# Kernel optimization log

Measured on AMD Instinct MI355X. Metric: run time of the kernel, lower is better.

## Reference

```python
import jax, jax.numpy as jnp
import numpy as np

N = 50000
E = 800000
IN_CH = 128
HID = 64
H1 = 4  # heads in gat1
NEG_SLOPE = 0.2


def _gat_layer(x, src, dst, W, a_src, a_dst, bias, heads, ch):
    # x: [N, F_in]; W: [F_in, heads*ch]; a_src/a_dst: [heads, ch]; bias: [heads*ch]
    n = x.shape[0]
    h = (x @ W).reshape(n, heads, ch)                       # [N, H, C]
    alpha_src = jnp.einsum('nhc,hc->nh', h, a_src)          # [N, H]
    alpha_dst = jnp.einsum('nhc,hc->nh', h, a_dst)          # [N, H]
    e = jax.nn.leaky_relu(alpha_src[src] + alpha_dst[dst], NEG_SLOPE)  # [E, H]
    # segment softmax over incoming edges of each destination node
    m = jax.ops.segment_max(e, dst, num_segments=n)         # [N, H]
    ex = jnp.exp(e - m[dst])                                # [E, H]
    denom = jax.ops.segment_sum(ex, dst, num_segments=n)    # [N, H]
    alpha = ex / (denom[dst] + 1e-16)                       # [E, H]
    out = jax.ops.segment_sum(alpha[:, :, None] * h[src], dst, num_segments=n)  # [N, H, C]
    return out.reshape(n, heads * ch) + bias


def setup_inputs() -> dict:
    key = jax.random.key(0)
    ks = jax.random.split(key, 12)
    x = jax.random.normal(ks[0], (N, IN_CH), dtype=jnp.float32)
    edge_index = jax.random.randint(ks[1], (2, E), 0, N, dtype=jnp.int64)
    s1 = 1.0 / np.sqrt(IN_CH)
    s2 = 1.0 / np.sqrt(H1 * HID)
    s3 = 1.0 / np.sqrt(HID)
    return {
        'x': x,
        'edge_index': edge_index,
        'W1': jax.random.uniform(ks[2], (IN_CH, H1 * HID), jnp.float32, -s1, s1),
        'att_src1': jax.random.uniform(ks[3], (H1, HID), jnp.float32, -s1, s1),
        'att_dst1': jax.random.uniform(ks[4], (H1, HID), jnp.float32, -s1, s1),
        'b1': jnp.zeros((H1 * HID,), jnp.float32),
        'W2': jax.random.uniform(ks[5], (H1 * HID, HID), jnp.float32, -s2, s2),
        'att_src2': jax.random.uniform(ks[6], (1, HID), jnp.float32, -s2, s2),
        'att_dst2': jax.random.uniform(ks[7], (1, HID), jnp.float32, -s2, s2),
        'b2': jnp.zeros((HID,), jnp.float32),
        'W_out': jax.random.uniform(ks[8], (HID, 1), jnp.float32, -s3, s3),
        'b_out': jnp.zeros((1,), jnp.float32),
    }


def reference(x, edge_index, W1, att_src1, att_dst1, b1, W2, att_src2, att_dst2, b2, W_out, b_out):
    # add self-loops (PyG GATConv default)
    loops = jnp.arange(N, dtype=edge_index.dtype)
    src = jnp.concatenate([edge_index[0], loops])
    dst = jnp.concatenate([edge_index[1], loops])
    h = jax.nn.relu(_gat_layer(x, src, dst, W1, att_src1, att_dst1, b1, H1, HID))
    h = jax.nn.relu(_gat_layer(h, src, dst, W2, att_src2, att_dst2, b2, 1, HID))
    return (h @ W_out + b_out).squeeze(-1)  # [N]
```

## Files before the change

### kernel.cpp

```cpp
#include <hip/hip_runtime.h>
#include <hip/hip_bf16.h>
#include <math.h>

#define N_NODES 50000
#define N_EDGES 800000
#define EE_TOTAL (N_EDGES + N_NODES)
#define CAP 64

#define GEMM1_BLOCKS ((N_NODES + 63) / 64)
#define SCAT_BLOCKS ((EE_TOTAL + 1023) / 1024)
#define FUSED_BLOCKS (GEMM1_BLOCKS + SCAT_BLOCKS)
#define AGG1_BLOCKS 25000

typedef __attribute__((ext_vector_type(8))) short bf16x8;
typedef __attribute__((ext_vector_type(4))) float f32x4;

__device__ __forceinline__ float bf2f(unsigned short s) {
  return __uint_as_float((unsigned)s << 16);
}
__device__ __forceinline__ unsigned short f2bf(float f) {
  unsigned u = __float_as_uint(f);
  return (unsigned short)((u + 0x7FFFu + ((u >> 16) & 1u)) >> 16);
}
__device__ __forceinline__ float lrelu(float e) { return e > 0.f ? e : 0.2f * e; }

__global__ void prep_kernel(const float* __restrict__ W1, const float* __restrict__ W2,
                            unsigned short* __restrict__ W1t, unsigned short* __restrict__ W2t,
                            int* __restrict__ counts) {
  int i = blockIdx.x * blockDim.x + threadIdx.x;
  if (i < N_NODES) counts[i] = 0;
  if (i < 256 * 128) W1t[i] = f2bf(W1[(i & 127) * 256 + (i >> 7)]);
  if (i < 64 * 256) W2t[i] = f2bf(W2[(i & 255) * 64 + (i >> 8)]);
}

__device__ __forceinline__ void scatter_body(int sid, int t,
                                             const int* __restrict__ src,
                                             const int* __restrict__ dst,
                                             int* __restrict__ counts,
                                             unsigned short* __restrict__ col) {
  int base = sid * 1024 + t * 4;
  int ss[4], dd[4];
#pragma unroll
  for (int k = 0; k < 4; ++k) {
    int i = base + k;
    if (i < N_EDGES) { ss[k] = src[i]; dd[k] = dst[i]; }
    else if (i < EE_TOTAL) { ss[k] = i - N_EDGES; dd[k] = ss[k]; }
    else { ss[k] = 0; dd[k] = -1; }
  }
#pragma unroll
  for (int k = 0; k < 4; ++k) {
    if (dd[k] >= 0) {
      int pos = atomicAdd(&counts[dd[k]], 1);
      if (pos < CAP) col[(size_t)dd[k] * CAP + pos] = (unsigned short)ss[k];
    }
  }
}

__global__ __launch_bounds__(256) void fused_kernel(const int* __restrict__ src,
                                                    const int* __restrict__ dst,
                                                    int* __restrict__ counts,
                                                    unsigned short* __restrict__ col,
                                                    const float* __restrict__ A,
                                                    const unsigned short* __restrict__ Bt,
                                                    unsigned short* __restrict__ Cb,
                                                    const float* __restrict__ att_s,
                                                    const float* __restrict__ att_d,
                                                    float* __restrict__ as_out,
                                                    float* __restrict__ ad_out) {
  __shared__ unsigned short Bs[256 * 128];
  int b = blockIdx.x;
  int t = threadIdx.x;
  bool is_gemm;
  int id;
  if (b < 2 * GEMM1_BLOCKS) { is_gemm = (b & 1) == 0; id = b >> 1; }
  else { is_gemm = false; id = b - GEMM1_BLOCKS; }

  if (!is_gemm) {
    scatter_body(id, t, src, dst, counts, col);
    return;
  }

  const int M = N_NODES;
  int lane = t & 63, w = t >> 6;
  int row0 = id * 64;
#pragma unroll
  for (int i = 0; i < 16; ++i) {
    int idx = i * 256 + t;
    int n = idx >> 4;
    uint4 v = ((const uint4*)Bt)[idx];
    int byte = (idx * 16) ^ ((n & 7) << 4);
    *(uint4*)((char*)Bs + byte) = v;
  }
  __syncthreads();
  int rl = lane & 15, kg = lane >> 4;
  f32x4 acc[4][4] = {};
  for (int ks = 0; ks < 4; ++ks) {
    bf16x8 af[4], bfr[4];
#pragma unroll
    for (int rb = 0; rb < 4; ++rb) {
      int row = row0 + rb * 16 + rl;
      float4 v0 = make_float4(0.f, 0.f, 0.f, 0.f), v1 = v0;
      if (row < M) {
        const float* p = A + (size_t)row * 128 + ks * 32 + kg * 8;
        v0 = *(const float4*)p;
        v1 = *(const float4*)(p + 4);
      }
      bf16x8 a;
      a[0] = (short)f2bf(v0.x); a[1] = (short)f2bf(v0.y);
      a[2] = (short)f2bf(v0.z); a[3] = (short)f2bf(v0.w);
      a[4] = (short)f2bf(v1.x); a[5] = (short)f2bf(v1.y);
      a[6] = (short)f2bf(v1.z); a[7] = (short)f2bf(v1.w);
      af[rb] = a;
    }
#pragma unroll
    for (int cb = 0; cb < 4; ++cb) {
      int n = w * 64 + cb * 16 + rl;
      int byte = (n * 256 + ks * 64 + kg * 16) ^ ((n & 7) << 4);
      bfr[cb] = *(const bf16x8*)((char*)Bs + byte);
    }
#pragma unroll
    for (int rb = 0; rb < 4; ++rb)
#pragma unroll
      for (int cb = 0; cb < 4; ++cb)
        acc[rb][cb] = __builtin_amdgcn_mfma_f32_16x16x32_bf16(af[rb], bfr[cb], acc[rb][cb], 0, 0, 0);
  }
  float asv[4], adv[4];
#pragma unroll
  for (int cb = 0; cb < 4; ++cb) {
    int c = w * 64 + cb * 16 + rl;
    asv[cb] = att_s[c];
    adv[cb] = att_d[c];
  }
#pragma unroll
  for (int rb = 0; rb < 4; ++rb) {
#pragma unroll
    for (int r = 0; r < 4; ++r) {
      int row = row0 + rb * 16 + kg * 4 + r;
      bool ok = row < M;
      float sp = 0.f, dp = 0.f;
#pragma unroll
      for (int cb = 0; cb < 4; ++cb) {
        float v = acc[rb][cb][r];
        if (ok) Cb[(size_t)row * 256 + w * 64 + cb * 16 + rl] = f2bf(v);
        sp += v * asv[cb];
        dp += v * adv[cb];
      }
#pragma unroll
      for (int off = 1; off < 16; off <<= 1) {
        sp += __shfl_xor(sp, off, 64);
        dp += __shfl_xor(dp, off, 64);
      }
      if (ok && rl == 0) {
        as_out[w * M + row] = sp;
        ad_out[w * M + row] = dp;
      }
    }
  }
}

__global__ __launch_bounds__(256) void gemm2_kernel(const unsigned short* __restrict__ A,
                                                    const unsigned short* __restrict__ Bt,
                                                    unsigned short* __restrict__ Cb,
                                                    const float* __restrict__ att_s,
                                                    const float* __restrict__ att_d,
                                                    float* __restrict__ as_out,
                                                    float* __restrict__ ad_out) {
  __shared__ unsigned short Bs[64 * 256];
  const int M = N_NODES;
  int t = threadIdx.x;
  int lane = t & 63, w = t >> 6;
  int row0 = blockIdx.x * 64;
#pragma unroll
  for (int i = 0; i < 8; ++i) {
    int idx = i * 256 + t;
    int n = idx >> 5;
    uint4 v = ((const uint4*)Bt)[idx];
    int byte = (idx * 16) ^ ((n & 7) << 4);
    *(uint4*)((char*)Bs + byte) = v;
  }
  __syncthreads();
  int rl = lane & 15, kg = lane >> 4;
  int arow = row0 + w * 16 + rl;
  f32x4 acc[4] = {};
  for (int ks = 0; ks < 8; ++ks) {
    bf16x8 a = {};
    if (arow < M) a = *(const bf16x8*)(A + (size_t)arow * 256 + ks * 32 + kg * 8);
#pragma unroll
    for (int cb = 0; cb < 4; ++cb) {
      int n = cb * 16 + rl;
      int byte = (n * 512 + ks * 64 + kg * 16) ^ ((n & 7) << 4);
      bf16x8 bfrag = *(const bf16x8*)((char*)Bs + byte);
      acc[cb] = __builtin_amdgcn_mfma_f32_16x16x32_bf16(a, bfrag, acc[cb], 0, 0, 0);
    }
  }
  float asv[4], adv[4];
#pragma unroll
  for (int cb = 0; cb < 4; ++cb) {
    int c = cb * 16 + rl;
    asv[cb] = att_s[c];
    adv[cb] = att_d[c];
  }
#pragma unroll
  for (int r = 0; r < 4; ++r) {
    int orow = row0 + w * 16 + kg * 4 + r;
    bool ok = orow < M;
    float sp = 0.f, dp = 0.f;
#pragma unroll
    for (int cb = 0; cb < 4; ++cb) {
      float v = acc[cb][r];
      if (ok) Cb[(size_t)orow * 64 + cb * 16 + rl] = f2bf(v);
      sp += v * asv[cb];
      dp += v * adv[cb];
    }
#pragma unroll
    for (int off = 1; off < 16; off <<= 1) {
      sp += __shfl_xor(sp, off, 64);
      dp += __shfl_xor(dp, off, 64);
    }
    if (ok && rl == 0) {
      as_out[orow] = sp;
      ad_out[orow] = dp;
    }
  }
}

__global__ __launch_bounds__(256) void agg1_kernel(const unsigned short* __restrict__ h1b,
                                                   const float* __restrict__ as_t,
                                                   const float* __restrict__ ad_t,
                                                   const int* __restrict__ counts,
                                                   const unsigned short* __restrict__ col,
                                                   const float* __restrict__ b1,
                                                   unsigned short* __restrict__ x2b) {
  __shared__ int s_lds[8][64];
  __shared__ float p_lds[8][64];
  const int M = N_NODES;
  int bid = blockIdx.x;
  int head = (bid & 7) >> 1;
  int idx = (bid >> 3) * 2 + (bid & 1);
  int t = threadIdx.x;
  int hw = t >> 5;
  int sl = t & 31;
  int node = idx * 8 + hw;
  int cnt = min(counts[node], CAP);
  const unsigned short* cbase = col + (size_t)node * CAP;
  const float* as_h = as_t + (size_t)head * M;
  float adn = ad_t[(size_t)head * M + node];
  float den = 0.f;
  {
    int e = sl;
    int s = node;
    float p = 0.f;
    if (e < cnt) {
      s = cbase[e];
      p = __expf(lrelu(as_h[s] + adn));
    }
    s_lds[hw][e] = s;
    p_lds[hw][e] = p;
    den += p;
  }
  if (cnt > 32) {
    int e = 32 + sl;
    int s = node;
    float p = 0.f;
    if (e < cnt) {
      s = cbase[e];
      p = __expf(lrelu(as_h[s] + adn));
    }
    s_lds[hw][e] = s;
    p_lds[hw][e] = p;
    den += p;
  }
#pragma unroll
  for (int off = 1; off < 32; off <<= 1) den += __shfl_xor(den, off, 64);
  int e_off = sl >> 3, cl = sl & 7;
  const unsigned short* hb = h1b + head * 64 + cl * 8;
  float acc[8] = {};
  int nq = (cnt + 3) & ~3;
  int sa = s_lds[hw][e_off];
  float pa = p_lds[hw][e_off];
  bf16x8 va = *(const bf16x8*)(hb + (size_t)sa * 256);
  for (int j = 4; j < nq; j += 4) {
    int sb = s_lds[hw][j + e_off];
    float pb = p_lds[hw][j + e_off];
    bf16x8 vb = *(const bf16x8*)(hb + (size_t)sb * 256);
#pragma unroll
    for (int k = 0; k < 8; ++k) acc[k] += pa * bf2f((unsigned short)va[k]);
    va = vb; pa = pb;
  }
#pragma unroll
  for (int k = 0; k < 8; ++k) acc[k] += pa * bf2f((unsigned short)va[k]);
#pragma unroll
  for (int k = 0; k < 8; ++k) {
    acc[k] += __shfl_xor(acc[k], 8, 64);
    acc[k] += __shfl_xor(acc[k], 16, 64);
  }
  if (e_off == 0) {
    float inv = 1.f / (den + 1e-16f);
    int ch = head * 64 + cl * 8;
    float4 blo = *(const float4*)(b1 + ch);
    float4 bhi = *(const float4*)(b1 + ch + 4);
    float bb[8] = {blo.x, blo.y, blo.z, blo.w, bhi.x, bhi.y, bhi.z, bhi.w};
    bf16x8 o;
#pragma unroll
    for (int k = 0; k < 8; ++k) o[k] = (short)f2bf(fmaxf(acc[k] * inv + bb[k], 0.f));
    *(bf16x8*)(x2b + (size_t)node * 256 + ch) = o;
  }
}

__global__ __launch_bounds__(256) void agg2_final_kernel(const unsigned short* __restrict__ h2b,
                                                         const float* __restrict__ as,
                                                         const float* __restrict__ ad,
                                                         const int* __restrict__ counts,
                                                         const unsigned short* __restrict__ col,
                                                         const float* __restrict__ b2,
                                                         const float* __restrict__ Wout,
                                                         const float* __restrict__ bout,
                                                         float* __restrict__ out) {
  __shared__ int s_lds[4][64];
  __shared__ float p_lds[4][64];
  int t = threadIdx.x;
  int lane = t & 63, w = t >> 6;
  int node = blockIdx.x * 4 + w;
  if (node >= N_NODES) return;
  int cnt = min(counts[node], CAP);
  const unsigned short* cbase = col + (size_t)node * CAP;
  float adn = ad[node];
  int g = lane >> 4, sl = lane & 15;
  int s = node;
  float p = 0.f;
  if (lane < cnt) {
    s = cbase[lane];
    p = __expf(lrelu(as[s] + adn));
  }
  s_lds[w][lane] = s;
  p_lds[w][lane] = p;
  float den = p;
#pragma unroll
  for (int off = 1; off < 64; off <<= 1) den += __shfl_xor(den, off, 64);
  float acc[4] = {};
  int nq = (cnt + 7) & ~7;
  for (int j = 0; j < nq; j += 8) {
    int e0 = j + g, e1 = j + 4 + g;
    int s0 = s_lds[w][e0], s1 = s_lds[w][e1];
    float p0 = p_lds[w][e0], p1 = p_lds[w][e1];
    ushort4 v0 = *(const ushort4*)(h2b + (size_t)s0 * 64 + sl * 4);
    ushort4 v1 = *(const ushort4*)(h2b + (size_t)s1 * 64 + sl * 4);
    acc[0] += p0 * bf2f(v0.x) + p1 * bf2f(v1.x);
    acc[1] += p0 * bf2f(v0.y) + p1 * bf2f(v1.y);
    acc[2] += p0 * bf2f(v0.z) + p1 * bf2f(v1.z);
    acc[3] += p0 * bf2f(v0.w) + p1 * bf2f(v1.w);
  }
#pragma unroll
  for (int k = 0; k < 4; ++k) {
    acc[k] += __shfl_xor(acc[k], 16, 64);
    acc[k] += __shfl_xor(acc[k], 32, 64);
  }
  float inv = 1.f / (den + 1e-16f);
  int ch = sl * 4;
  float4 b4 = *(const float4*)(b2 + ch);
  float4 w4 = *(const float4*)(Wout + ch);
  float part = fmaxf(acc[0] * inv + b4.x, 0.f) * w4.x +
               fmaxf(acc[1] * inv + b4.y, 0.f) * w4.y +
               fmaxf(acc[2] * inv + b4.z, 0.f) * w4.z +
               fmaxf(acc[3] * inv + b4.w, 0.f) * w4.w;
#pragma unroll
  for (int off = 1; off < 16; off <<= 1) part += __shfl_xor(part, off, 64);
  if (lane == 0) out[node] = part + bout[0];
}

extern "C" void kernel_launch(void* const* d_in, const int* in_sizes, int n_in,
                              void* d_out, int out_size, void* d_ws, size_t ws_size,
                              hipStream_t stream) {
  const float* x    = (const float*)d_in[0];
  const int*   ei   = (const int*)d_in[1];
  const float* W1   = (const float*)d_in[2];
  const float* as1w = (const float*)d_in[3];
  const float* ad1w = (const float*)d_in[4];
  const float* b1   = (const float*)d_in[5];
  const float* W2   = (const float*)d_in[6];
  const float* as2w = (const float*)d_in[7];
  const float* ad2w = (const float*)d_in[8];
  const float* b2   = (const float*)d_in[9];
  const float* Wout = (const float*)d_in[10];
  const float* bout = (const float*)d_in[11];
  float* out = (float*)d_out;

  const int* src = ei;
  const int* dst = ei + N_EDGES;

  char* ws = (char*)d_ws;
  size_t off = 0;
  auto alloc = [&](size_t bytes) -> char* {
    char* p = ws + off;
    off += (bytes + 255) & ~(size_t)255;
    return p;
  };
  int*            counts = (int*)alloc((size_t)N_NODES * 4);
  unsigned short* col    = (unsigned short*)alloc((size_t)N_NODES * CAP * 2);
  unsigned short* W1t    = (unsigned short*)alloc((size_t)256 * 128 * 2);
  unsigned short* W2t    = (unsigned short*)alloc((size_t)64 * 256 * 2);
  unsigned short* x2b    = (unsigned short*)alloc((size_t)N_NODES * 256 * 2);
  unsigned short* hbuf   = (unsigned short*)alloc((size_t)N_NODES * 256 * 2);
  float*          as1    = (float*)alloc((size_t)N_NODES * 4 * 4);
  float*          ad1    = (float*)alloc((size_t)N_NODES * 4 * 4);
  float*          as2    = (float*)alloc((size_t)N_NODES * 4);
  float*          ad2    = (float*)alloc((size_t)N_NODES * 4);

  unsigned short* h1b = hbuf;
  unsigned short* h2b = hbuf;

  const int node_blocks4 = (N_NODES + 3) / 4;
  const int gemm_blocks = (N_NODES + 63) / 64;

  prep_kernel<<<(N_NODES + 255) / 256, 256, 0, stream>>>(W1, W2, W1t, W2t, counts);

  fused_kernel<<<FUSED_BLOCKS, 256, 0, stream>>>(src, dst, counts, col,
                                                 x, W1t, h1b, as1w, ad1w, as1, ad1);

  agg1_kernel<<<AGG1_BLOCKS, 256, 0, stream>>>(h1b, as1, ad1, counts, col, b1, x2b);

  gemm2_kernel<<<gemm_blocks, 256, 0, stream>>>(x2b, W2t, h2b, as2w, ad2w, as2, ad2);
  agg2_final_kernel<<<node_blocks4, 256, 0, stream>>>(h2b, as2, ad2, counts, col, b2,
                                                      Wout, bout, out);
}
```

Baseline: 151.5 us.

## Store layer-1 features in half-head planar layout to localize agg1 gathers

The first GEMM now writes its bf16 output into eight planar slices (one per half-head of 32 channels), each holding all nodes contiguously, in place of row-major 256-wide rows. The layer-1 aggregation kernel is reorganised so each block handles one half-head for 16 nodes, with 16 lanes per node, and gathers 64-byte rows from a compact per-slice array. The aim is better cache locality for random neighbor gathers, since each block's working set is one 3.2 MB slice. The cost is that attention scores and softmax denominators are recomputed for both halves of each head, and the GEMM epilogue stores are more scattered.

```diff
diff --git a/kernel.cpp b/kernel.cpp
--- a/kernel.cpp
+++ b/kernel.cpp
@@ -62,7 +62,7 @@
                                                     unsigned short* __restrict__ col,
                                                     const float* __restrict__ A,
                                                     const unsigned short* __restrict__ Bt,
-                                                    unsigned short* __restrict__ Cb,
+                                                    unsigned short* __restrict__ h1t,
                                                     const float* __restrict__ att_s,
                                                     const float* __restrict__ att_d,
                                                     float* __restrict__ as_out,
@@ -141,7 +141,10 @@
 #pragma unroll
       for (int cb = 0; cb < 4; ++cb) {
         float v = acc[rb][cb][r];
-        if (ok) Cb[(size_t)row * 256 + w * 64 + cb * 16 + rl] = f2bf(v);
+        if (ok) {
+          size_t hc = (size_t)(w * 2 + (cb >> 1));
+          h1t[(hc * M + row) * 32 + (cb & 1) * 16 + rl] = f2bf(v);
+        }
         sp += v * asv[cb];
         dp += v * adv[cb];
       }
@@ -224,65 +227,56 @@
   }
 }
 
-__global__ __launch_bounds__(256) void agg1_kernel(const unsigned short* __restrict__ h1b,
+__global__ __launch_bounds__(256) void agg1_kernel(const unsigned short* __restrict__ h1t,
                                                    const float* __restrict__ as_t,
                                                    const float* __restrict__ ad_t,
                                                    const int* __restrict__ counts,
                                                    const unsigned short* __restrict__ col,
                                                    const float* __restrict__ b1,
                                                    unsigned short* __restrict__ x2b) {
-  __shared__ int s_lds[8][64];
-  __shared__ float p_lds[8][64];
+  __shared__ int s_lds[16][64];
+  __shared__ float p_lds[16][64];
   const int M = N_NODES;
   int bid = blockIdx.x;
-  int head = (bid & 7) >> 1;
-  int idx = (bid >> 3) * 2 + (bid & 1);
+  int hc = bid & 7;
+  int head = hc >> 1, chh = hc & 1;
   int t = threadIdx.x;
-  int hw = t >> 5;
-  int sl = t & 31;
-  int node = idx * 8 + hw;
+  int qw = t >> 4;
+  int sl = t & 15;
+  int node = (bid >> 3) * 16 + qw;
   int cnt = min(counts[node], CAP);
   const unsigned short* cbase = col + (size_t)node * CAP;
   const float* as_h = as_t + (size_t)head * M;
   float adn = ad_t[(size_t)head * M + node];
+  int nq = (cnt + 3) & ~3;
   float den = 0.f;
-  {
-    int e = sl;
-    int s = node;
-    float p = 0.f;
-    if (e < cnt) {
-      s = cbase[e];
-      p = __expf(lrelu(as_h[s] + adn));
-    }
-    s_lds[hw][e] = s;
-    p_lds[hw][e] = p;
-    den += p;
-  }
-  if (cnt > 32) {
-    int e = 32 + sl;
-    int s = node;
-    float p = 0.f;
-    if (e < cnt) {
-      s = cbase[e];
-      p = __expf(lrelu(as_h[s] + adn));
-    }
-    s_lds[hw][e] = s;
-    p_lds[hw][e] = p;
-    den += p;
-  }
-#pragma unroll
-  for (int off = 1; off < 32; off <<= 1) den += __shfl_xor(den, off, 64);
-  int e_off = sl >> 3, cl = sl & 7;
-  const unsigned short* hb = h1b + head * 64 + cl * 8;
+#pragma unroll
+  for (int r = 0; r < 4; ++r) {
+    if (r == 0 || r * 16 < nq) {
+      int e = r * 16 + sl;
+      int s = node;
+      float p = 0.f;
+      if (e < cnt) {
+        s = cbase[e];
+        p = __expf(lrelu(as_h[s] + adn));
+      }
+      s_lds[qw][e] = s;
+      p_lds[qw][e] = p;
+      den += p;
+    }
+  }
+#pragma unroll
+  for (int off = 1; off < 16; off <<= 1) den += __shfl_xor(den, off, 64);
+  int e_off = sl >> 2, cl = sl & 3;
+  const unsigned short* hb = h1t + (size_t)hc * M * 32 + cl * 8;
   float acc[8] = {};
-  int nq = (cnt + 3) & ~3;
-  int sa = s_lds[hw][e_off];
-  float pa = p_lds[hw][e_off];
-  bf16x8 va = *(const bf16x8*)(hb + (size_t)sa * 256);
+  int sa = s_lds[qw][e_off];
+  float pa = p_lds[qw][e_off];
+  bf16x8 va = *(const bf16x8*)(hb + (size_t)sa * 32);
   for (int j = 4; j < nq; j += 4) {
-    int sb = s_lds[hw][j + e_off];
-    float pb = p_lds[hw][j + e_off];
-    bf16x8 vb = *(const bf16x8*)(hb + (size_t)sb * 256);
+    int sb = s_lds[qw][j + e_off];
+    float pb = p_lds[qw][j + e_off];
+    bf16x8 vb = *(const bf16x8*)(hb + (size_t)sb * 32);
 #pragma unroll
     for (int k = 0; k < 8; ++k) acc[k] += pa * bf2f((unsigned short)va[k]);
     va = vb; pa = pb;
@@ -291,12 +285,12 @@
   for (int k = 0; k < 8; ++k) acc[k] += pa * bf2f((unsigned short)va[k]);
 #pragma unroll
   for (int k = 0; k < 8; ++k) {
+    acc[k] += __shfl_xor(acc[k], 4, 64);
     acc[k] += __shfl_xor(acc[k], 8, 64);
-    acc[k] += __shfl_xor(acc[k], 16, 64);
   }
   if (e_off == 0) {
     float inv = 1.f / (den + 1e-16f);
-    int ch = head * 64 + cl * 8;
+    int ch = head * 64 + chh * 32 + cl * 8;
     float4 blo = *(const float4*)(b1 + ch);
     float4 bhi = *(const float4*)(b1 + ch + 4);
     float bb[8] = {blo.x, blo.y, blo.z, blo.w, bhi.x, bhi.y, bhi.z, bhi.w};
@@ -406,7 +400,7 @@
   float*          as2    = (float*)alloc((size_t)N_NODES * 4);
   float*          ad2    = (float*)alloc((size_t)N_NODES * 4);
 
-  unsigned short* h1b = hbuf;
+  unsigned short* h1t = hbuf;
   unsigned short* h2b = hbuf;
 
   const int node_blocks4 = (N_NODES + 3) / 4;
@@ -415,9 +409,9 @@
   prep_kernel<<<(N_NODES + 255) / 256, 256, 0, stream>>>(W1, W2, W1t, W2t, counts);
 
   fused_kernel<<<FUSED_BLOCKS, 256, 0, stream>>>(src, dst, counts, col,
-                                                 x, W1t, h1b, as1w, ad1w, as1, ad1);
-
-  agg1_kernel<<<AGG1_BLOCKS, 256, 0, stream>>>(h1b, as1, ad1, counts, col, b1, x2b);
+                                                 x, W1t, h1t, as1w, ad1w, as1, ad1);
+
+  agg1_kernel<<<AGG1_BLOCKS, 256, 0, stream>>>(h1t, as1, ad1, counts, col, b1, x2b);
 
   gemm2_kernel<<<gemm_blocks, 256, 0, stream>>>(x2b, W2t, h2b, as2w, ad2w, as2, ad2);
   agg2_final_kernel<<<node_blocks4, 256, 0, stream>>>(h2b, as2, ad2, counts, col, b2,
```

Measured after the change: 169.7 us. +12.0%, slower.
